# Optimization experiments

Measured on AMD Instinct MI355X. Metric: run time of the kernel, lower is better.

The kernel has to match this reference:

```python
import jax, jax.numpy as jnp
import numpy as np

SIGMA = 0.1  # init kwarg sigma
B_CONST = 1.0  # init kwarg b
EPS = 1e-5


def setup_inputs() -> dict:
    key = jax.random.key(0)
    k1, k2 = jax.random.split(key)
    shape = (4, 256, 48, 48)  # N, C, H, W
    return {
        "featureT": jax.random.normal(k1, shape, dtype=jnp.float32),
        "featureI": jax.random.normal(k2, shape, dtype=jnp.float32),
    }


def reference(featureT, featureI):
    # center both features by the target's per-channel mean (over N, H, W)
    meanT = featureT.mean(axis=(0, 2, 3), keepdims=True)
    fI = featureI - meanT
    fT = featureT - meanT
    # l2-normalize channelwise (dim=1)
    fI = fI / jnp.linalg.norm(fI, axis=1, keepdims=True)
    fT = fT / jnp.linalg.norm(fT, axis=1, keepdims=True)
    N, C, H, W = fT.shape
    P = H * W
    # per-sample all-pairs patch cosine similarity: dist[n,p,h,w] = sum_c fT[n,c,p] * fI[n,c,h,w]
    # (equivalent to the per-sample F.conv2d with 1x1 filters from patch_decomposition)
    dist = jnp.einsum('ncp,nchw->nphw', fT.reshape(N, C, P), fI)  # [N, P, H, W]
    raw_dist = (1.0 - dist) / 2.0
    # relative distances along the patch axis (axis=1)
    div = jnp.min(raw_dist, axis=1, keepdims=True)
    relative_dist = raw_dist / (div + EPS)
    # contextual similarity: exp-weighted normalization along axis=1
    Wmat = jnp.exp((B_CONST - relative_dist) / SIGMA)
    CX = Wmat / jnp.sum(Wmat, axis=1, keepdims=True)
    # max over spatial dims (3 then 2), mean over patches
    CX = CX.max(axis=(2, 3))  # [N, P]
    CX = CX.mean(axis=1)      # [N]
    CX_B = -jnp.log(CX)       # [N]
    loss = jnp.mean(CX_B)
    return (loss, CX_B)
```

## Files before the change

### kernel.cpp

```cpp
#include <hip/hip_runtime.h>
#include <hip/hip_fp16.h>

#define NN 4
#define CC 256
#define PP 2304
#define EPSV 1e-5f

typedef __attribute__((ext_vector_type(8))) short bf16x8;
typedef __attribute__((ext_vector_type(4))) float f32x4;

struct alignas(8) h4 { __half2 a, b; };
struct alignas(16) h8 { __half2 a, b, c, d; };

__device__ inline unsigned fenc(float f) {
  unsigned b = __float_as_uint(f);
  return (b & 0x80000000u) ? ~b : (b | 0x80000000u);
}
__device__ inline float fdec(unsigned e) {
  unsigned b = (e & 0x80000000u) ? (e ^ 0x80000000u) : ~e;
  return __uint_as_float(b);
}

__device__ inline unsigned short f2bf(float x) {
  unsigned u = __float_as_uint(x);
  unsigned r = (u + 0x7FFFu + ((u >> 16) & 1u)) >> 16;
  return (unsigned short)r;
}

__device__ inline void gload_lds16(const unsigned short* g, unsigned short* l) {
  __builtin_amdgcn_global_load_lds(
      (const __attribute__((address_space(1))) void*)g,
      (__attribute__((address_space(3))) void*)l, 16, 0, 0);
}

__global__ __launch_bounds__(256) void k_mean(const float* __restrict__ fT,
                                              float* __restrict__ partial,
                                              unsigned* __restrict__ divu,
                                              float* __restrict__ cxsum) {
  int c = blockIdx.x, n = blockIdx.y, t = threadIdx.x;
  const float4* base = (const float4*)(fT + ((size_t)n * CC + c) * PP);
  float s = 0.f;
  for (int k = t; k < 576; k += 256) {
    float4 v = base[k];
    s += (v.x + v.y) + (v.z + v.w);
  }
  for (int o = 32; o > 0; o >>= 1) s += __shfl_down(s, o);
  __shared__ float red[4];
  if ((t & 63) == 0) red[t >> 6] = s;
  __syncthreads();
  if (t == 0) partial[c * NN + n] = red[0] + red[1] + red[2] + red[3];
  if (n == 0 && t < 36) divu[c * 36 + t] = 0xFFFFFFFFu;
  if (n == 0 && c == 0 && t < 4) cxsum[t] = 0.f;
}

__global__ __launch_bounds__(256) void k_norm(const float* __restrict__ fT,
                                              const float* __restrict__ fI,
                                              const float* __restrict__ partial,
                                              unsigned short* __restrict__ A,
                                              unsigned short* __restrict__ B) {
  int n = blockIdx.y;
  int p0 = blockIdx.x * 16;
  int t = threadIdx.x;
  int pq = (t & 3) * 4;
  int cg = t >> 2;
  __shared__ float cT[16][257];
  __shared__ float cI[16][257];
  __shared__ float redf[2][16][65];
  __shared__ float inv[2][16];
  float aT[4] = {0.f, 0.f, 0.f, 0.f}, aI[4] = {0.f, 0.f, 0.f, 0.f};
#pragma unroll
  for (int ph = 0; ph < 4; ph++) {
    int c = ph * 64 + cg;
    float m = (partial[c * NN + 0] + partial[c * NN + 1] +
               partial[c * NN + 2] + partial[c * NN + 3]) * (1.0f / (float)(NN * PP));
    size_t g = ((size_t)n * CC + c) * PP + p0 + pq;
    float4 vT = *(const float4*)(fT + g);
    float4 vI = *(const float4*)(fI + g);
    float xT[4] = {vT.x - m, vT.y - m, vT.z - m, vT.w - m};
    float xI[4] = {vI.x - m, vI.y - m, vI.z - m, vI.w - m};
#pragma unroll
    for (int k = 0; k < 4; k++) {
      cT[pq + k][c] = xT[k]; cI[pq + k][c] = xI[k];
      aT[k] += xT[k] * xT[k]; aI[k] += xI[k] * xI[k];
    }
  }
#pragma unroll
  for (int k = 0; k < 4; k++) {
    redf[0][pq + k][cg] = aT[k];
    redf[1][pq + k][cg] = aI[k];
  }
  __syncthreads();
  if (t < 32) {
    int which = t >> 4, p = t & 15;
    float s = 0.f;
    for (int g = 0; g < 64; g++) s += redf[which][p][g];
    inv[which][p] = 1.0f / sqrtf(s);
  }
  __syncthreads();
#pragma unroll
  for (int it = 0; it < 2; it++) {
    int task = it * 256 + t;
    int ps = task >> 5;
    int ch = task & 31;
    float iA = inv[0][ps], iB = inv[1][ps];
    unsigned short va[8], vb[8];
#pragma unroll
    for (int e = 0; e < 8; e++) {
      va[e] = f2bf(cT[ps][ch * 8 + e] * iA);
      vb[e] = f2bf(cI[ps][ch * 8 + e] * iB);
    }
    size_t o = ((size_t)(n * PP + p0 + ps)) * CC + ch * 8;
    *(int4*)(A + o) = *(const int4*)va;
    *(int4*)(B + o) = *(const int4*)vb;
  }
}

__global__ __launch_bounds__(256) void k_gemm(const unsigned short* __restrict__ A,
                                              const unsigned short* __restrict__ B,
                                              __half* __restrict__ rawt,
                                              unsigned* __restrict__ divu) {
  int n  = blockIdx.z;
  int i0 = blockIdx.y * 128;
  int j0 = blockIdx.x * 128;
  int t  = threadIdx.x;
  int lane = t & 63;
  int w = t >> 6;
  int wi = w >> 1, wj = w & 1;
  int lr = lane & 15, lq = lane >> 4;

  __shared__ __align__(16) char smem[33792];
  unsigned short* As = (unsigned short*)smem;
  unsigned short* Bs = (unsigned short*)(smem + 16384);
  __half* r16t = (__half*)smem;
  __shared__ unsigned cmin[128];
  if (t < 128) cmin[t] = 0xFFFFFFFFu;

  f32x4 acc[4][4];
#pragma unroll
  for (int a = 0; a < 4; a++)
#pragma unroll
    for (int b = 0; b < 4; b++) acc[a][b] = (f32x4){0.f, 0.f, 0.f, 0.f};

  const size_t baseA = ((size_t)(n * PP + i0)) * CC;
  const size_t baseB = ((size_t)(n * PP + j0)) * CC;
  int lrow8 = lane >> 3;
  int lseg  = (lane & 7) ^ (lrow8 & 7);

  for (int k0 = 0; k0 < CC; k0 += 64) {
    if (k0) __syncthreads();
#pragma unroll
    for (int it = 0; it < 4; it++) {
      int sb = (w * 4 + it) * 64;
      int row = (w * 4 + it) * 8 + lrow8;
      gload_lds16(A + baseA + (size_t)row * CC + k0 + lseg * 8, As + sb * 8);
      gload_lds16(B + baseB + (size_t)row * CC + k0 + lseg * 8, Bs + sb * 8);
    }
    __syncthreads();
#pragma unroll
    for (int ks = 0; ks < 2; ks++) {
      bf16x8 af[4], bf[4];
#pragma unroll
      for (int ti = 0; ti < 4; ti++) {
        int row = wi * 64 + ti * 16 + lr;
        int slot = row * 8 + ((ks * 4 + lq) ^ (lr & 7));
        af[ti] = *(const bf16x8*)&As[slot * 8];
      }
#pragma unroll
      for (int tj = 0; tj < 4; tj++) {
        int row = wj * 64 + tj * 16 + lr;
        int slot = row * 8 + ((ks * 4 + lq) ^ (lr & 7));
        bf[tj] = *(const bf16x8*)&Bs[slot * 8];
      }
#pragma unroll
      for (int ti = 0; ti < 4; ti++)
#pragma unroll
        for (int tj = 0; tj < 4; tj++)
          acc[ti][tj] = __builtin_amdgcn_mfma_f32_16x16x32_bf16(af[ti], bf[tj], acc[ti][tj], 0, 0, 0);
    }
  }

  __syncthreads();
#pragma unroll
  for (int tj = 0; tj < 4; tj++) {
    float mx = -1e30f;
    int cj = wj * 64 + tj * 16 + lr;
#pragma unroll
    for (int ti = 0; ti < 4; ti++) {
      alignas(8) unsigned short pk[4];
#pragma unroll
      for (int r = 0; r < 4; r++) {
        float g = acc[ti][tj][r];
        mx = fmaxf(mx, g);
        pk[r] = __half_as_ushort(__float2half((1.0f - g) * 0.5f));
      }
      int ci = wi * 64 + ti * 16 + lq * 4;
      *(short4*)&r16t[cj * 132 + ci] = *(const short4*)pk;
    }
    atomicMin(&cmin[cj], fenc((1.0f - mx) * 0.5f));
  }
  __syncthreads();
#pragma unroll
  for (int m = 0; m < 8; m++) {
    int chunk = m * 256 + t;
    int row = chunk >> 4, cs = chunk & 15;
    int2 lo = *(const int2*)&r16t[row * 132 + cs * 8];
    int2 hi = *(const int2*)&r16t[row * 132 + cs * 8 + 4];
    int4 v = {lo.x, lo.y, hi.x, hi.y};
    *(int4*)(rawt + ((size_t)(n * PP + j0 + row)) * PP + i0 + cs * 8) = v;
  }
  if (t < 128) atomicMin(&divu[n * PP + j0 + t], cmin[t]);
}

__global__ __launch_bounds__(256) void k_colsum(const __half* __restrict__ rawt,
                                                const unsigned* __restrict__ divu,
                                                float* __restrict__ scale,
                                                float* __restrict__ lnS) {
  int t = threadIdx.x, lane = t & 63, w = t >> 6;
  int r = blockIdx.x * 4 + w;
  float d = fdec(divu[r]);
  float sc = -10.0f / (d + EPSV);
  const __half* rp = rawt + (size_t)r * PP;
  float s = 0.f;
#pragma unroll
  for (int c = 0; c < 4; c++) {
    h8 hv = *(const h8*)(rp + c * 512 + lane * 8);
    float2 f0 = __half22float2(hv.a), f1 = __half22float2(hv.b);
    float2 f2 = __half22float2(hv.c), f3 = __half22float2(hv.d);
    s += __expf(f0.x * sc) + __expf(f0.y * sc) + __expf(f1.x * sc) + __expf(f1.y * sc);
    s += __expf(f2.x * sc) + __expf(f2.y * sc) + __expf(f3.x * sc) + __expf(f3.y * sc);
  }
  {
    h4 hv = *(const h4*)(rp + 2048 + lane * 4);
    float2 f01 = __half22float2(hv.a), f23 = __half22float2(hv.b);
    s += __expf(f01.x * sc) + __expf(f01.y * sc) + __expf(f23.x * sc) + __expf(f23.y * sc);
  }
  for (int o = 32; o > 0; o >>= 1) s += __shfl_down(s, o);
  if (lane == 0) {
    scale[r] = sc;
    lnS[r] = logf(s);
  }
}

__global__ __launch_bounds__(512) void k_rowmax(const __half* __restrict__ rawt,
                                                const float* __restrict__ scale,
                                                const float* __restrict__ lnS,
                                                float* __restrict__ cxsum) {
  int n = blockIdx.y;
  int i0 = blockIdx.x * 32;
  int t = threadIdx.x, lane = t & 63, w = t >> 6;
  int q = t & 7, g = t >> 3;
  int i = i0 + q * 4;
  const float* scp = scale + n * PP;
  const float* lnp = lnS + n * PP;
  float m0 = -1e30f, m1 = -1e30f, m2 = -1e30f, m3 = -1e30f;
#pragma unroll 4
  for (int it = 0; it < 36; it++) {
    int j = it * 64 + g;
    float scj = scp[j], lsj = lnp[j];
    h4 hv = *(const h4*)(rawt + ((size_t)(n * PP + j)) * PP + i);
    float2 f01 = __half22float2(hv.a);
    float2 f23 = __half22float2(hv.b);
    m0 = fmaxf(m0, fmaf(f01.x, scj, -lsj));
    m1 = fmaxf(m1, fmaf(f01.y, scj, -lsj));
    m2 = fmaxf(m2, fmaf(f23.x, scj, -lsj));
    m3 = fmaxf(m3, fmaf(f23.y, scj, -lsj));
  }
#pragma unroll
  for (int o = 8; o <= 32; o <<= 1) {
    m0 = fmaxf(m0, __shfl_xor(m0, o));
    m1 = fmaxf(m1, __shfl_xor(m1, o));
    m2 = fmaxf(m2, __shfl_xor(m2, o));
    m3 = fmaxf(m3, __shfl_xor(m3, o));
  }
  __shared__ float4 red[8][8];
  if (lane < 8) red[w][lane] = (float4){m0, m1, m2, m3};
  __syncthreads();
  if (t < 8) {
    float4 a = red[0][t];
#pragma unroll
    for (int ww = 1; ww < 8; ww++) {
      float4 b = red[ww][t];
      a.x = fmaxf(a.x, b.x); a.y = fmaxf(a.y, b.y);
      a.z = fmaxf(a.z, b.z); a.w = fmaxf(a.w, b.w);
    }
    float v = (__expf(a.x) + __expf(a.y) + __expf(a.z) + __expf(a.w)) * (1.0f / (float)PP);
    v += __shfl_down(v, 4);
    v += __shfl_down(v, 2);
    v += __shfl_down(v, 1);
    if (t == 0) atomicAdd(&cxsum[n], v);
  }
}

__global__ void k_final(const float* __restrict__ cxsum, float* __restrict__ out) {
  int t = threadIdx.x;
  float cxb = 0.f;
  if (t < 4) {
    cxb = -logf(cxsum[t]);
    out[1 + t] = cxb;
  }
  for (int o = 2; o > 0; o >>= 1) cxb += __shfl_down(cxb, o);
  if (t == 0) out[0] = cxb * 0.25f;
}

extern "C" void kernel_launch(void* const* d_in, const int* in_sizes, int n_in,
                              void* d_out, int out_size, void* d_ws, size_t ws_size,
                              hipStream_t stream) {
  const float* fT = (const float*)d_in[0];
  const float* fI = (const float*)d_in[1];
  float* out = (float*)d_out;

  char* w = (char*)d_ws;
  float* partial = (float*)w;
  unsigned* divu = (unsigned*)(w + 4096);
  float* scale   = (float*)(w + 4096 + 36864);
  float* lnS     = (float*)(w + 4096 + 2 * 36864);
  float* cxsum   = (float*)(w + 4096 + 3 * 36864);
  size_t off = 4096 + 3 * 36864 + 1024;
  unsigned short* A = (unsigned short*)(w + off);
  unsigned short* B = (unsigned short*)(w + off + 4718592);
  __half* rawt = (__half*)(w + off + 2 * 4718592);

  k_mean<<<dim3(CC, NN), 256, 0, stream>>>(fT, partial, divu, cxsum);
  k_norm<<<dim3(PP / 16, NN), 256, 0, stream>>>(fT, fI, partial, A, B);
  k_gemm<<<dim3(PP / 128, PP / 128, NN), 256, 0, stream>>>(A, B, rawt, divu);
  k_colsum<<<dim3(PP * NN / 4), 256, 0, stream>>>(rawt, divu, scale, lnS);
  k_rowmax<<<dim3(PP / 32, NN), 512, 0, stream>>>(rawt, scale, lnS, cxsum);
  k_final<<<1, 64, 0, stream>>>(cxsum, out);
}
```

Baseline: 123.5 us.

## Split row-max over j-chunks with atomicMax and add separate exp-sum kernel

The row-max pass now tiles 256 columns per block and splits the 2304-row reduction into 24 chunks along a third grid dimension. Partial maxima are merged in global memory with atomicMax on order-preserving encoded floats, and a new kernel applies exp and sums into cxsum. The aim is wider, more coalesced row reads (64 lanes times 4 halves) and more parallelism. The cost is an extra launch, many global atomics and a workspace layout shift.

```diff
diff --git a/kernel.cpp b/kernel.cpp
--- a/kernel.cpp
+++ b/kernel.cpp
@@ -36,6 +36,7 @@
 __global__ __launch_bounds__(256) void k_mean(const float* __restrict__ fT,
                                               float* __restrict__ partial,
                                               unsigned* __restrict__ divu,
+                                              unsigned* __restrict__ M,
                                               float* __restrict__ cxsum) {
   int c = blockIdx.x, n = blockIdx.y, t = threadIdx.x;
   const float4* base = (const float4*)(fT + ((size_t)n * CC + c) * PP);
@@ -49,7 +50,11 @@
   if ((t & 63) == 0) red[t >> 6] = s;
   __syncthreads();
   if (t == 0) partial[c * NN + n] = red[0] + red[1] + red[2] + red[3];
-  if (n == 0 && t < 36) divu[c * 36 + t] = 0xFFFFFFFFu;
+  if (n == 0 && t < 36) {
+    int idx = c * 36 + t;
+    divu[idx] = 0xFFFFFFFFu;
+    M[idx] = 0u;
+  }
   if (n == 0 && c == 0 && t < 4) cxsum[t] = 0.f;
 }
 
@@ -241,54 +246,54 @@
   }
 }
 
-__global__ __launch_bounds__(512) void k_rowmax(const __half* __restrict__ rawt,
+__global__ __launch_bounds__(256) void k_rowmax(const __half* __restrict__ rawt,
                                                 const float* __restrict__ scale,
                                                 const float* __restrict__ lnS,
-                                                float* __restrict__ cxsum) {
+                                                unsigned* __restrict__ M) {
   int n = blockIdx.y;
-  int i0 = blockIdx.x * 32;
-  int t = threadIdx.x, lane = t & 63, w = t >> 6;
-  int q = t & 7, g = t >> 3;
-  int i = i0 + q * 4;
-  const float* scp = scale + n * PP;
-  const float* lnp = lnS + n * PP;
-  float m0 = -1e30f, m1 = -1e30f, m2 = -1e30f, m3 = -1e30f;
-#pragma unroll 4
-  for (int it = 0; it < 36; it++) {
-    int j = it * 64 + g;
-    float scj = scp[j], lsj = lnp[j];
+  int i0 = blockIdx.x * 256;
+  int rz = blockIdx.z;
+  int t = threadIdx.x;
+  int lane = t & 63, w = t >> 6;
+  int i = i0 + lane * 4;
+
+  float4 m = {-1e30f, -1e30f, -1e30f, -1e30f};
+  int j0 = rz * 96;
+  for (int j = j0 + w; j < j0 + 96; j += 4) {
+    float scj = scale[n * PP + j];
+    float lsj = lnS[n * PP + j];
     h4 hv = *(const h4*)(rawt + ((size_t)(n * PP + j)) * PP + i);
     float2 f01 = __half22float2(hv.a);
     float2 f23 = __half22float2(hv.b);
-    m0 = fmaxf(m0, fmaf(f01.x, scj, -lsj));
-    m1 = fmaxf(m1, fmaf(f01.y, scj, -lsj));
-    m2 = fmaxf(m2, fmaf(f23.x, scj, -lsj));
-    m3 = fmaxf(m3, fmaf(f23.y, scj, -lsj));
-  }
-#pragma unroll
-  for (int o = 8; o <= 32; o <<= 1) {
-    m0 = fmaxf(m0, __shfl_xor(m0, o));
-    m1 = fmaxf(m1, __shfl_xor(m1, o));
-    m2 = fmaxf(m2, __shfl_xor(m2, o));
-    m3 = fmaxf(m3, __shfl_xor(m3, o));
-  }
-  __shared__ float4 red[8][8];
-  if (lane < 8) red[w][lane] = (float4){m0, m1, m2, m3};
-  __syncthreads();
-  if (t < 8) {
-    float4 a = red[0][t];
-#pragma unroll
-    for (int ww = 1; ww < 8; ww++) {
-      float4 b = red[ww][t];
-      a.x = fmaxf(a.x, b.x); a.y = fmaxf(a.y, b.y);
-      a.z = fmaxf(a.z, b.z); a.w = fmaxf(a.w, b.w);
-    }
-    float v = (__expf(a.x) + __expf(a.y) + __expf(a.z) + __expf(a.w)) * (1.0f / (float)PP);
-    v += __shfl_down(v, 4);
-    v += __shfl_down(v, 2);
-    v += __shfl_down(v, 1);
-    if (t == 0) atomicAdd(&cxsum[n], v);
-  }
+    m.x = fmaxf(m.x, fmaf(f01.x, scj, -lsj));
+    m.y = fmaxf(m.y, fmaf(f01.y, scj, -lsj));
+    m.z = fmaxf(m.z, fmaf(f23.x, scj, -lsj));
+    m.w = fmaxf(m.w, fmaf(f23.y, scj, -lsj));
+  }
+  __shared__ float4 red4[4][64];
+  red4[w][lane] = m;
+  __syncthreads();
+  if (t < 64) {
+    float4 a = red4[0][t], b = red4[1][t], c = red4[2][t], d = red4[3][t];
+    int ii = i0 + t * 4;
+    atomicMax(&M[n * PP + ii + 0], fenc(fmaxf(fmaxf(a.x, b.x), fmaxf(c.x, d.x))));
+    atomicMax(&M[n * PP + ii + 1], fenc(fmaxf(fmaxf(a.y, b.y), fmaxf(c.y, d.y))));
+    atomicMax(&M[n * PP + ii + 2], fenc(fmaxf(fmaxf(a.z, b.z), fmaxf(c.z, d.z))));
+    atomicMax(&M[n * PP + ii + 3], fenc(fmaxf(fmaxf(a.w, b.w), fmaxf(c.w, d.w))));
+  }
+}
+
+__global__ __launch_bounds__(256) void k_cx(const unsigned* __restrict__ M,
+                                            float* __restrict__ cxsum) {
+  int b = blockIdx.x, t = threadIdx.x;
+  int idx = b * 256 + t;
+  int n = idx / PP;
+  float v = __expf(fdec(M[idx])) * (1.0f / (float)PP);
+  for (int o = 32; o > 0; o >>= 1) v += __shfl_down(v, o);
+  __shared__ float red[4];
+  if ((t & 63) == 0) red[t >> 6] = v;
+  __syncthreads();
+  if (t == 0) atomicAdd(&cxsum[n], red[0] + red[1] + red[2] + red[3]);
 }
 
 __global__ void k_final(const float* __restrict__ cxsum, float* __restrict__ out) {
@@ -314,16 +319,18 @@
   unsigned* divu = (unsigned*)(w + 4096);
   float* scale   = (float*)(w + 4096 + 36864);
   float* lnS     = (float*)(w + 4096 + 2 * 36864);
-  float* cxsum   = (float*)(w + 4096 + 3 * 36864);
-  size_t off = 4096 + 3 * 36864 + 1024;
+  unsigned* M    = (unsigned*)(w + 4096 + 3 * 36864);
+  float* cxsum   = (float*)(w + 4096 + 4 * 36864);
+  size_t off = 4096 + 4 * 36864 + 1024;
   unsigned short* A = (unsigned short*)(w + off);
   unsigned short* B = (unsigned short*)(w + off + 4718592);
   __half* rawt = (__half*)(w + off + 2 * 4718592);
 
-  k_mean<<<dim3(CC, NN), 256, 0, stream>>>(fT, partial, divu, cxsum);
+  k_mean<<<dim3(CC, NN), 256, 0, stream>>>(fT, partial, divu, M, cxsum);
   k_norm<<<dim3(PP / 16, NN), 256, 0, stream>>>(fT, fI, partial, A, B);
   k_gemm<<<dim3(PP / 128, PP / 128, NN), 256, 0, stream>>>(A, B, rawt, divu);
   k_colsum<<<dim3(PP * NN / 4), 256, 0, stream>>>(rawt, divu, scale, lnS);
-  k_rowmax<<<dim3(PP / 32, NN), 512, 0, stream>>>(rawt, scale, lnS, cxsum);
+  k_rowmax<<<dim3(PP / 256, NN, 24), 256, 0, stream>>>(rawt, scale, lnS, M);
+  k_cx<<<36, 256, 0, stream>>>(M, cxsum);
   k_final<<<1, 64, 0, stream>>>(cxsum, out);
 }
```

After: 123.7 us. About the same (+0.2%).
